# Performance work log

Measured on AMD Instinct MI355X. Metric: run time of the kernel, lower is better.

The kernel has to match this reference:

```python
import math
import jax, jax.numpy as jnp
import numpy as np

CH = 256
NUM_GROUPS = 32
EPS = 1e-5


def setup_inputs() -> dict:
    key = jax.random.key(0)
    ks = jax.random.split(key, 8)
    B, C, S = 32, CH, 32
    x = jax.random.normal(ks[0], (B, C, S, S), dtype=jnp.float32)
    t_embd = jax.random.normal(ks[1], (B, 4 * C), dtype=jnp.float32)
    gamma = jnp.ones((C,), dtype=jnp.float32)
    beta = jnp.zeros((C,), dtype=jnp.float32)
    # torch nn.Linear(ch, 3*ch): weight shape (3*ch, ch), y = x @ W.T + b
    w_attn = jax.random.normal(ks[2], (3 * C, C), dtype=jnp.float32) * (1.0 / math.sqrt(C))
    b_attn = jax.random.normal(ks[3], (3 * C,), dtype=jnp.float32) * 0.02
    w_proj = jax.random.normal(ks[4], (C, C), dtype=jnp.float32) * (1.0 / math.sqrt(C))
    b_proj = jax.random.normal(ks[5], (C,), dtype=jnp.float32) * 0.02
    return {
        "x": x, "t_embd": t_embd,
        "gamma": gamma, "beta": beta,
        "w_attn": w_attn, "b_attn": b_attn,
        "w_proj": w_proj, "b_proj": b_proj,
    }


def _group_norm(x, gamma, beta):
    # x: (B, C, S, S), normalize over (C/G, S, S) per group
    B, C, S, _ = x.shape
    xg = x.reshape(B, NUM_GROUPS, (C // NUM_GROUPS) * S * S)
    mean = jnp.mean(xg, axis=-1, keepdims=True)
    var = jnp.var(xg, axis=-1, keepdims=True)
    xn = ((xg - mean) * jax.lax.rsqrt(var + EPS)).reshape(B, C, S, S)
    return xn * gamma[None, :, None, None] + beta[None, :, None, None]


def reference(x, t_embd, gamma, beta, w_attn, b_attn, w_proj, b_proj):
    B, C, S, _ = x.shape
    norm_x = _group_norm(x, gamma, beta)
    h = jnp.transpose(norm_x, (0, 2, 3, 1))            # (B, S, S, C)
    qkv = h @ w_attn.T + b_attn                        # (B, S, S, 3C)
    q, k, v = jnp.split(qkv, 3, axis=3)
    # full spatial attention: scores over all S*S key positions
    att = jnp.einsum('bhwc,bHWc->bhwHW', q, k) * (1.0 / math.sqrt(C))
    att = jax.nn.softmax(att.reshape(B, S, S, S * S), axis=-1).reshape(B, S, S, S, S)
    o = jnp.einsum('bhwHW,bHWc->bhwc', att, v)         # (B, S, S, C)
    y = o @ w_proj.T + b_proj
    y = jnp.transpose(y, (0, 3, 1, 2))                 # (B, C, S, S)
    return x + y
```

## Files before the change

### kernel.cpp

```cpp
#include <hip/hip_runtime.h>
#include <hip/hip_bf16.h>
#include <stdint.h>
#include <stddef.h>


typedef float  f32x4  __attribute__((ext_vector_type(4)));
typedef __bf16 bf16x8 __attribute__((ext_vector_type(8)));
typedef __bf16 bf16x4 __attribute__((ext_vector_type(4)));

#define DEVI static __device__ __forceinline__

DEVI f32x4 mfma16(bf16x8 a, bf16x8 b, f32x4 c) {
  return __builtin_amdgcn_mfma_f32_16x16x32_bf16(a, b, c, 0, 0, 0);
}

DEVI f32x4 zero4() { f32x4 z = {0.f, 0.f, 0.f, 0.f}; return z; }

typedef const __attribute__((address_space(1))) void* gas_cvp;
typedef __attribute__((address_space(3))) void*       las_vp;

DEVI void gl_lds16(const __bf16* g, __bf16* l) {
  __builtin_amdgcn_global_load_lds((gas_cvp)g, (las_vp)l, 16, 0, 0);
}

#define WAIT_VM(N) asm volatile("s_waitcnt vmcnt(" #N ")" ::: "memory")
DEVI void bar() {
  asm volatile("" ::: "memory");
  __builtin_amdgcn_s_barrier();
  asm volatile("" ::: "memory");
}

__global__ __launch_bounds__(256) void cvt_weights(
    const float* __restrict__ wa, const float* __restrict__ wp,
    __bf16* __restrict__ wab, __bf16* __restrict__ wpb) {
  const int i = blockIdx.x * 256 + threadIdx.x;
  if (i < 196608) {
    wab[i] = (__bf16)wa[i];
  } else {
    const int j = i - 196608;
    if (j < 65536) wpb[j] = (__bf16)wp[j];
  }
}

__global__ __launch_bounds__(256) void gn_fused(
    const float* __restrict__ x, const float* __restrict__ gamma,
    const float* __restrict__ beta, __bf16* __restrict__ h) {
  __shared__ __align__(16) float xs[8192];
  __shared__ float redS[4], redSS[4];
  const int bg = blockIdx.x;
  const int b = bg >> 5, g = bg & 31;
  const int tid = threadIdx.x;
  const float* base = x + (size_t)bg * 8192;
  float s = 0.f, ss = 0.f;
#pragma unroll
  for (int it = 0; it < 8; ++it) {
    const int i = it * 256 + tid;
    f32x4 v = *(const f32x4*)(base + i * 4);
    *(f32x4*)(xs + i * 4) = v;
    s  += v[0] + v[1] + v[2] + v[3];
    ss += v[0]*v[0] + v[1]*v[1] + v[2]*v[2] + v[3]*v[3];
  }
#pragma unroll
  for (int m = 1; m < 64; m <<= 1) {
    s  += __shfl_xor(s,  m, 64);
    ss += __shfl_xor(ss, m, 64);
  }
  const int lane = tid & 63, wave = tid >> 6;
  if (lane == 0) { redS[wave] = s; redSS[wave] = ss; }
  __syncthreads();
  const float S  = redS[0] + redS[1] + redS[2] + redS[3];
  const float SS = redSS[0] + redSS[1] + redSS[2] + redSS[3];
  const float mu = S * (1.f / 8192.f);
  const float rstd = rsqrtf(SS * (1.f / 8192.f) - mu * mu + 1e-5f);
  float ga[8], be[8];
#pragma unroll
  for (int j = 0; j < 8; ++j) {
    const int c = g * 8 + j;
    ga[j] = gamma[c] * rstd;
    be[j] = beta[c] - mu * ga[j];
  }
  __bf16* hb = h + ((size_t)b << 18) + g * 8;
#pragma unroll
  for (int it = 0; it < 4; ++it) {
    const int p = it * 256 + tid;
    bf16x8 o8;
#pragma unroll
    for (int j = 0; j < 8; ++j)
      o8[j] = (__bf16)(xs[j * 1024 + p] * ga[j] + be[j]);
    *(bf16x8*)(hb + ((size_t)p << 8)) = o8;
  }
}

DEVI void gemm_core_k256(const __bf16* __restrict__ A0, const __bf16* __restrict__ B0,
                         __bf16* lA, __bf16* lB, int lane, int wave, f32x4 acc[4][4]) {
  const int wm = (wave >> 1) * 64;
  const int wn = (wave & 1) * 64;
  const int r15 = lane & 15, lg = lane >> 4;
#pragma unroll
  for (int i = 0; i < 4; ++i)
#pragma unroll
    for (int j = 0; j < 4; ++j) acc[i][j] = zero4();

  for (int ko = 0; ko < 4; ++ko) {
#pragma unroll
    for (int it = 0; it < 4; ++it) {
      const int q = wave * 256 + it * 64 + lane;
      const int row = q >> 3, c8 = q & 7;
      const int srcoff = row * 256 + ko * 64 + ((c8 ^ (row & 7)) << 3);
      gl_lds16(A0 + srcoff, lA + (size_t)(wave * 256 + it * 64) * 8);
      gl_lds16(B0 + srcoff, lB + (size_t)(wave * 256 + it * 64) * 8);
    }
    __syncthreads();
#pragma unroll
    for (int kk = 0; kk < 2; ++kk) {
      bf16x8 af[4], bfr[4];
#pragma unroll
      for (int i = 0; i < 4; ++i) {
        const int row = wm + i * 16 + r15;
        af[i] = *(const bf16x8*)((const char*)lA + row * 128 +
                                 (((kk * 4 + lg) ^ (row & 7)) << 4));
      }
#pragma unroll
      for (int j = 0; j < 4; ++j) {
        const int row = wn + j * 16 + r15;
        bfr[j] = *(const bf16x8*)((const char*)lB + row * 128 +
                                  (((kk * 4 + lg) ^ (row & 7)) << 4));
      }
#pragma unroll
      for (int i = 0; i < 4; ++i)
#pragma unroll
        for (int j = 0; j < 4; ++j) acc[i][j] = mfma16(af[i], bfr[j], acc[i][j]);
    }
    __syncthreads();
  }
}

__global__ __launch_bounds__(256) void qkv_gemm(
    const __bf16* __restrict__ h, const __bf16* __restrict__ wab,
    const float* __restrict__ b_attn,
    __bf16* __restrict__ q, __bf16* __restrict__ k, __bf16* __restrict__ vt) {
  __shared__ __align__(16) __bf16 lA[128 * 64], lB[128 * 64];
  const int nt = blockIdx.x, mt = blockIdx.y;
  const int tid = threadIdx.x, lane = tid & 63, wave = tid >> 6;
  f32x4 acc[4][4];
  gemm_core_k256(h + (size_t)mt * 128 * 256, wab + (size_t)nt * 128 * 256,
                 lA, lB, lane, wave, acc);

  const int wm = (wave >> 1) * 64, wn = (wave & 1) * 64;
  const int r15 = lane & 15, lg = lane >> 4;
  const int sec = nt >> 1;
  const float QS = 0.0625f * 1.44269504088896340736f;
#pragma unroll
  for (int j = 0; j < 4; ++j) {
    const int ng = nt * 128 + wn + j * 16 + r15;
    const float bias = b_attn[ng];
    const int c = ng & 255;
#pragma unroll
    for (int i = 0; i < 4; ++i) {
      const int mbase = mt * 128 + wm + i * 16 + lg * 4;
      if (sec == 0) {
#pragma unroll
        for (int r = 0; r < 4; ++r)
          q[(size_t)(mbase + r) * 256 + c] = (__bf16)((acc[i][j][r] + bias) * QS);
      } else if (sec == 1) {
#pragma unroll
        for (int r = 0; r < 4; ++r)
          k[(size_t)(mbase + r) * 256 + c] = (__bf16)(acc[i][j][r] + bias);
      } else {
        const int b = mbase >> 10, p = mbase & 1023;
        bf16x4 pk;
#pragma unroll
        for (int r = 0; r < 4; ++r) pk[r] = (__bf16)(acc[i][j][r] + bias);
        *(bf16x4*)(vt + (((size_t)(b * 256 + c)) << 10) + p) = pk;
      }
    }
  }
}

__global__ __launch_bounds__(256, 2) void attn(
    const __bf16* __restrict__ q, const __bf16* __restrict__ k,
    const __bf16* __restrict__ vt, __bf16* __restrict__ o) {
  extern __shared__ __align__(16) char smem[];

  const int bid = blockIdx.x;
  const int xcd = bid & 7, sub = bid >> 3;
  const int b = xcd * 4 + (sub & 3);
  const int qt = sub >> 2;
  const int tid = threadIdx.x, lane = tid & 63, wave = tid >> 6;
  const int r15 = lane & 15, lg = lane >> 4, rs7 = r15 & 7;
  const int m0 = qt * 64 + wave * 16;
  char* P = smem + 65536 + wave * 2048;

  const __bf16* kb = k  + ((size_t)b << 18);
  const __bf16* vb = vt + ((size_t)b << 18);

  const __bf16* qb = q + (((size_t)(b * 1024 + m0)) << 8);
  bf16x8 qf[8];
#pragma unroll
  for (int kc = 0; kc < 8; ++kc)
    qf[kc] = *(const bf16x8*)(qb + ((size_t)r15) * 256 + kc * 32 + lg * 8);

  f32x4 po[16];
#pragma unroll
  for (int d = 0; d < 16; ++d) po[d] = zero4();
  float mrun = -1e30f, lrun = 0.f;

  auto stageK = [&](int n0) {
    __bf16* dst = (__bf16*)smem;
#pragma unroll
    for (int it = 0; it < 8; ++it) {
      const int qch = it * 256 + tid;
      const int row = qch >> 5, c32 = qch & 31;
      gl_lds16(kb + (size_t)(n0 + row) * 256 + ((c32 ^ (row & 7)) << 3),
               dst + (size_t)(it * 256 + wave * 64) * 8);
    }
  };
  auto stageV = [&](int n0) {
    __bf16* dst = (__bf16*)(smem + 32768);
#pragma unroll
    for (int it = 0; it < 8; ++it) {
      const int qch = it * 256 + tid;
      const int row = qch >> 3, c8 = qch & 7;
      gl_lds16(vb + ((size_t)row << 10) + n0 + ((c8 ^ (row & 7)) << 3),
               dst + (size_t)(it * 256 + wave * 64) * 8);
    }
  };

  stageK(0);
  stageV(0);

  const char* lK = (const char*)smem;
  const char* lV = (const char*)smem + 32768;

  for (int kv = 0; kv < 16; ++kv) {
    WAIT_VM(8);
    bar();

    f32x4 s[4];
#pragma unroll
    for (int j = 0; j < 4; ++j) s[j] = zero4();
    __builtin_amdgcn_s_setprio(1);
#pragma unroll
    for (int kc = 0; kc < 8; ++kc) {
      bf16x8 kf[4];
#pragma unroll
      for (int j = 0; j < 4; ++j)
        kf[j] = *(const bf16x8*)(lK + (j * 16 + r15) * 512 +
                                 (((kc * 4 + lg) ^ rs7) << 4));
#pragma unroll
      for (int j = 0; j < 4; ++j) s[j] = mfma16(kf[j], qf[kc], s[j]);
    }
    __builtin_amdgcn_s_setprio(0);
    float pmax = s[0][0];
#pragma unroll
    for (int j = 0; j < 4; ++j)
#pragma unroll
      for (int r = 0; r < 4; ++r) pmax = fmaxf(pmax, s[j][r]);
    pmax = fmaxf(pmax, __shfl_xor(pmax, 16, 64));
    pmax = fmaxf(pmax, __shfl_xor(pmax, 32, 64));
    if (!__all(pmax <= mrun + 8.f)) {
      const float mn = fmaxf(mrun, pmax);
      const float scl = exp2f(mrun - mn);
      mrun = mn;
      lrun *= scl;
#pragma unroll
      for (int d = 0; d < 16; ++d) po[d] *= scl;
    }
    float psum = 0.f;
    bf16x4 pk[4];
#pragma unroll
    for (int j = 0; j < 4; ++j)
#pragma unroll
      for (int r = 0; r < 4; ++r) {
        const float pv = exp2f(s[j][r] - mrun);
        psum += pv;
        pk[j][r] = (__bf16)pv;
      }
    psum += __shfl_xor(psum, 16, 64);
    psum += __shfl_xor(psum, 32, 64);
    lrun += psum;
#pragma unroll
    for (int j = 0; j < 4; ++j)
      *(bf16x4*)(P + r15 * 128 + ((j * 32 + lg * 8) ^ (rs7 << 4))) = pk[j];

    WAIT_VM(0);
    bar();
    if (kv < 15) stageK((kv + 1) * 64);

    __builtin_amdgcn_s_setprio(1);
#pragma unroll
    for (int kk = 0; kk < 2; ++kk) {
      const bf16x8 pb =
          *(const bf16x8*)(P + r15 * 128 + (((kk * 4 + lg) ^ rs7) << 4));
#pragma unroll
      for (int df = 0; df < 16; ++df) {
        const bf16x8 vf = *(const bf16x8*)(lV + (df * 16 + r15) * 128 +
                                           (((kk * 4 + lg) ^ rs7) << 4));
        po[df] = mfma16(vf, pb, po[df]);
      }
    }
    __builtin_amdgcn_s_setprio(0);
    bar();
    if (kv < 15) stageV((kv + 1) * 64);
  }
  const float inv = 1.f / lrun;
  __bf16* ob = o + (((size_t)(b * 1024 + m0 + r15)) << 8);
#pragma unroll
  for (int df = 0; df < 16; ++df) {
    bf16x4 t;
#pragma unroll
    for (int r = 0; r < 4; ++r) t[r] = (__bf16)(po[df][r] * inv);
    *(bf16x4*)(ob + df * 16 + lg * 4) = t;
  }
}

__global__ __launch_bounds__(256) void proj_gemm(
    const __bf16* __restrict__ o, const __bf16* __restrict__ wpb,
    const float* __restrict__ b_proj, const float* __restrict__ x,
    float* __restrict__ out) {
  __shared__ __align__(16) __bf16 lA[128 * 64], lB[128 * 64];
  const int nt = blockIdx.x, mt = blockIdx.y;
  const int tid = threadIdx.x, lane = tid & 63, wave = tid >> 6;
  f32x4 acc[4][4];
  gemm_core_k256(o + (size_t)mt * 128 * 256, wpb + (size_t)nt * 128 * 256,
                 lA, lB, lane, wave, acc);

  const int wm = (wave >> 1) * 64, wn = (wave & 1) * 64;
  const int r15 = lane & 15, lg = lane >> 4;
#pragma unroll
  for (int j = 0; j < 4; ++j) {
    const int c = nt * 128 + wn + j * 16 + r15;
    const float bias = b_proj[c];
#pragma unroll
    for (int i = 0; i < 4; ++i) {
      const int mbase = mt * 128 + wm + i * 16 + lg * 4;
      const int b = mbase >> 10, p = mbase & 1023;
      const size_t off = (((size_t)(b * 256 + c)) << 10) + p;
      f32x4 xv = *(const f32x4*)(x + off);
      f32x4 r = acc[i][j];
      r = r + xv;
      r = r + bias;
      *(f32x4*)(out + off) = r;
    }
  }
}

extern "C" void kernel_launch(void* const* d_in, const int* in_sizes, int n_in,
                              void* d_out, int out_size, void* d_ws, size_t ws_size,
                              hipStream_t stream) {
  const float* x      = (const float*)d_in[0];
  const float* gamma  = (const float*)d_in[2];
  const float* beta   = (const float*)d_in[3];
  const float* w_attn = (const float*)d_in[4];
  const float* b_attn = (const float*)d_in[5];
  const float* w_proj = (const float*)d_in[6];
  const float* b_proj = (const float*)d_in[7];
  float* out = (float*)d_out;

  char* ws = (char*)d_ws;
  __bf16* h   = (__bf16*)(ws);
  __bf16* qb  = (__bf16*)(ws + ((size_t)16 << 20));
  __bf16* kb  = (__bf16*)(ws + ((size_t)32 << 20));
  __bf16* vtb = (__bf16*)(ws + ((size_t)48 << 20));
  __bf16* wab = (__bf16*)(ws + ((size_t)64 << 20));
  __bf16* wpb = wab + 196608;

  cvt_weights<<<1024, 256, 0, stream>>>(w_attn, w_proj, wab, wpb);
  gn_fused<<<1024, 256, 0, stream>>>(x, gamma, beta, h);
  qkv_gemm<<<dim3(6, 256), 256, 0, stream>>>(h, wab, b_attn, qb, kb, vtb);
  attn<<<512, 256, 73728, stream>>>(qb, kb, vtb, h );
  proj_gemm<<<dim3(2, 256), 256, 0, stream>>>(h, wpb, b_proj, x, out);
}
```

Before: 128.6 us.

## Split KV range across two wave groups per block with 32-row query tiles

```diff
diff --git a/kernel.cpp b/kernel.cpp
--- a/kernel.cpp
+++ b/kernel.cpp
@@ -177,7 +177,7 @@
   }
 }
 
-__global__ __launch_bounds__(256, 2) void attn(
+__global__ __launch_bounds__(512, 2) void attn(
     const __bf16* __restrict__ q, const __bf16* __restrict__ k,
     const __bf16* __restrict__ vt, __bf16* __restrict__ o) {
   extern __shared__ __align__(16) char smem[];
@@ -187,130 +187,178 @@
   const int b = xcd * 4 + (sub & 3);
   const int qt = sub >> 2;
   const int tid = threadIdx.x, lane = tid & 63, wave = tid >> 6;
+  const int w4 = wave & 3, grp = wave >> 2;
+  const int gtid = tid & 255;
   const int r15 = lane & 15, lg = lane >> 4, rs7 = r15 & 7;
-  const int m0 = qt * 64 + wave * 16;
-  char* P = smem + 65536 + wave * 2048;
+  const int m0 = qt * 128 + w4 * 32;
+  char* KB = smem + grp * 16384;
+  char* VB = smem + 32768 + grp * 16384;
+  char* P  = smem + 65536 + wave * 2048;
 
   const __bf16* kb = k  + ((size_t)b << 18);
   const __bf16* vb = vt + ((size_t)b << 18);
-
-  const __bf16* qb = q + (((size_t)(b * 1024 + m0)) << 8);
-  bf16x8 qf[8];
-#pragma unroll
-  for (int kc = 0; kc < 8; ++kc)
-    qf[kc] = *(const bf16x8*)(qb + ((size_t)r15) * 256 + kc * 32 + lg * 8);
-
-  f32x4 po[16];
-#pragma unroll
-  for (int d = 0; d < 16; ++d) po[d] = zero4();
-  float mrun = -1e30f, lrun = 0.f;
+  const int kvbase = grp * 512;
+
+  const __bf16* qbp = q + (((size_t)(b * 1024 + m0)) << 8);
+  bf16x8 qf[2][8];
+#pragma unroll
+  for (int qh = 0; qh < 2; ++qh)
+#pragma unroll
+    for (int kc = 0; kc < 8; ++kc)
+      qf[qh][kc] = *(const bf16x8*)(qbp + (size_t)(qh * 16 + r15) * 256 + kc * 32 + lg * 8);
+
+  f32x4 po[16][2];
+#pragma unroll
+  for (int d = 0; d < 16; ++d)
+#pragma unroll
+    for (int qh = 0; qh < 2; ++qh) po[d][qh] = zero4();
+  float mrun[2] = {-1e30f, -1e30f}, lrun[2] = {0.f, 0.f};
 
   auto stageK = [&](int n0) {
-    __bf16* dst = (__bf16*)smem;
-#pragma unroll
-    for (int it = 0; it < 8; ++it) {
-      const int qch = it * 256 + tid;
+    __bf16* dst = (__bf16*)KB;
+#pragma unroll
+    for (int it = 0; it < 4; ++it) {
+      const int qch = it * 256 + gtid;
       const int row = qch >> 5, c32 = qch & 31;
       gl_lds16(kb + (size_t)(n0 + row) * 256 + ((c32 ^ (row & 7)) << 3),
-               dst + (size_t)(it * 256 + wave * 64) * 8);
+               dst + (size_t)(it * 256 + w4 * 64) * 8);
     }
   };
   auto stageV = [&](int n0) {
-    __bf16* dst = (__bf16*)(smem + 32768);
-#pragma unroll
-    for (int it = 0; it < 8; ++it) {
-      const int qch = it * 256 + tid;
-      const int row = qch >> 3, c8 = qch & 7;
-      gl_lds16(vb + ((size_t)row << 10) + n0 + ((c8 ^ (row & 7)) << 3),
-               dst + (size_t)(it * 256 + wave * 64) * 8);
+    __bf16* dst = (__bf16*)VB;
+#pragma unroll
+    for (int it = 0; it < 4; ++it) {
+      const int qch = it * 256 + gtid;
+      const int row = qch >> 2, c4 = qch & 3;
+      gl_lds16(vb + ((size_t)row << 10) + n0 + ((c4 ^ (row & 3)) << 3),
+               dst + (size_t)(it * 256 + w4 * 64) * 8);
     }
   };
 
-  stageK(0);
-  stageV(0);
-
-  const char* lK = (const char*)smem;
-  const char* lV = (const char*)smem + 32768;
-
-  for (int kv = 0; kv < 16; ++kv) {
-    WAIT_VM(8);
+  stageK(kvbase);
+  stageV(kvbase);
+
+  for (int t = 0; t < 16; ++t) {
+    const int n0n = kvbase + (t + 1) * 32;
+    WAIT_VM(4);
     bar();
 
-    f32x4 s[4];
-#pragma unroll
-    for (int j = 0; j < 4; ++j) s[j] = zero4();
+    f32x4 s[2][2];
+#pragma unroll
+    for (int qh = 0; qh < 2; ++qh)
+#pragma unroll
+      for (int j = 0; j < 2; ++j) s[qh][j] = zero4();
     __builtin_amdgcn_s_setprio(1);
 #pragma unroll
     for (int kc = 0; kc < 8; ++kc) {
-      bf16x8 kf[4];
-#pragma unroll
-      for (int j = 0; j < 4; ++j)
-        kf[j] = *(const bf16x8*)(lK + (j * 16 + r15) * 512 +
+      bf16x8 kf[2];
+#pragma unroll
+      for (int j = 0; j < 2; ++j)
+        kf[j] = *(const bf16x8*)(KB + (j * 16 + r15) * 512 +
                                  (((kc * 4 + lg) ^ rs7) << 4));
 #pragma unroll
-      for (int j = 0; j < 4; ++j) s[j] = mfma16(kf[j], qf[kc], s[j]);
+      for (int qh = 0; qh < 2; ++qh)
+#pragma unroll
+        for (int j = 0; j < 2; ++j) s[qh][j] = mfma16(kf[j], qf[qh][kc], s[qh][j]);
     }
     __builtin_amdgcn_s_setprio(0);
-    float pmax = s[0][0];
-#pragma unroll
-    for (int j = 0; j < 4; ++j)
-#pragma unroll
-      for (int r = 0; r < 4; ++r) pmax = fmaxf(pmax, s[j][r]);
-    pmax = fmaxf(pmax, __shfl_xor(pmax, 16, 64));
-    pmax = fmaxf(pmax, __shfl_xor(pmax, 32, 64));
-    if (!__all(pmax <= mrun + 8.f)) {
-      const float mn = fmaxf(mrun, pmax);
-      const float scl = exp2f(mrun - mn);
-      mrun = mn;
-      lrun *= scl;
-#pragma unroll
-      for (int d = 0; d < 16; ++d) po[d] *= scl;
-    }
-    float psum = 0.f;
-    bf16x4 pk[4];
-#pragma unroll
-    for (int j = 0; j < 4; ++j)
-#pragma unroll
-      for (int r = 0; r < 4; ++r) {
-        const float pv = exp2f(s[j][r] - mrun);
-        psum += pv;
-        pk[j][r] = (__bf16)pv;
-      }
-    psum += __shfl_xor(psum, 16, 64);
-    psum += __shfl_xor(psum, 32, 64);
-    lrun += psum;
-#pragma unroll
-    for (int j = 0; j < 4; ++j)
-      *(bf16x4*)(P + r15 * 128 + ((j * 32 + lg * 8) ^ (rs7 << 4))) = pk[j];
+    bf16x4 pk[2][2];
+#pragma unroll
+    for (int qh = 0; qh < 2; ++qh) {
+      float pmax = s[qh][0][0];
+#pragma unroll
+      for (int j = 0; j < 2; ++j)
+#pragma unroll
+        for (int r = 0; r < 4; ++r) pmax = fmaxf(pmax, s[qh][j][r]);
+      pmax = fmaxf(pmax, __shfl_xor(pmax, 16, 64));
+      pmax = fmaxf(pmax, __shfl_xor(pmax, 32, 64));
+      if (!__all(pmax <= mrun[qh] + 8.f)) {
+        const float mn = fmaxf(mrun[qh], pmax);
+        const float scl = exp2f(mrun[qh] - mn);
+        mrun[qh] = mn;
+        lrun[qh] *= scl;
+#pragma unroll
+        for (int d = 0; d < 16; ++d) po[d][qh] *= scl;
+      }
+      float psum = 0.f;
+#pragma unroll
+      for (int j = 0; j < 2; ++j)
+#pragma unroll
+        for (int r = 0; r < 4; ++r) {
+          const float pv = exp2f(s[qh][j][r] - mrun[qh]);
+          psum += pv;
+          pk[qh][j][r] = (__bf16)pv;
+        }
+      psum += __shfl_xor(psum, 16, 64);
+      psum += __shfl_xor(psum, 32, 64);
+      lrun[qh] += psum;
+    }
+#pragma unroll
+    for (int qh = 0; qh < 2; ++qh)
+#pragma unroll
+      for (int j = 0; j < 2; ++j) {
+        const int prow = qh * 16 + r15;
+        const int slot = (j * 2 + (lg >> 1)) ^ (prow & 3);
+        *(bf16x4*)(P + prow * 64 + (slot << 4) + ((lg & 1) * 8)) = pk[qh][j];
+      }
 
     WAIT_VM(0);
     bar();
-    if (kv < 15) stageK((kv + 1) * 64);
-
+    if (t < 15) stageK(n0n);
+
+    bf16x8 pb[2];
+#pragma unroll
+    for (int qh = 0; qh < 2; ++qh) {
+      const int prow = qh * 16 + r15;
+      pb[qh] = *(const bf16x8*)(P + prow * 64 + ((lg ^ (prow & 3)) << 4));
+    }
     __builtin_amdgcn_s_setprio(1);
 #pragma unroll
-    for (int kk = 0; kk < 2; ++kk) {
-      const bf16x8 pb =
-          *(const bf16x8*)(P + r15 * 128 + (((kk * 4 + lg) ^ rs7) << 4));
-#pragma unroll
-      for (int df = 0; df < 16; ++df) {
-        const bf16x8 vf = *(const bf16x8*)(lV + (df * 16 + r15) * 128 +
-                                           (((kk * 4 + lg) ^ rs7) << 4));
-        po[df] = mfma16(vf, pb, po[df]);
-      }
+    for (int df = 0; df < 16; ++df) {
+      const int vrow = df * 16 + r15;
+      const bf16x8 vf = *(const bf16x8*)(VB + vrow * 64 + ((lg ^ (vrow & 3)) << 4));
+#pragma unroll
+      for (int qh = 0; qh < 2; ++qh) po[df][qh] = mfma16(vf, pb[qh], po[df][qh]);
     }
     __builtin_amdgcn_s_setprio(0);
     bar();
-    if (kv < 15) stageV((kv + 1) * 64);
-  }
-  const float inv = 1.f / lrun;
-  __bf16* ob = o + (((size_t)(b * 1024 + m0 + r15)) << 8);
-#pragma unroll
-  for (int df = 0; df < 16; ++df) {
-    bf16x4 t;
-#pragma unroll
-    for (int r = 0; r < 4; ++r) t[r] = (__bf16)(po[df][r] * inv);
-    *(bf16x4*)(ob + df * 16 + lg * 4) = t;
+    if (t < 15) stageV(n0n);
+  }
+
+  if (grp == 1) {
+    f32x4 ml = {mrun[0], mrun[1], lrun[0], lrun[1]};
+    *(f32x4*)(smem + 65536 + ((w4 * 64 + lane) << 4)) = ml;
+#pragma unroll
+    for (int qh = 0; qh < 2; ++qh)
+#pragma unroll
+      for (int df = 0; df < 16; ++df) {
+        bf16x4 t;
+#pragma unroll
+        for (int r = 0; r < 4; ++r) t[r] = (__bf16)(po[df][qh][r]);
+        *(bf16x4*)(smem + w4 * 16384 + (qh * 16 + df) * 512 + lane * 8) = t;
+      }
+  }
+  bar();
+  if (grp == 0) {
+    const f32x4 ml = *(const f32x4*)(smem + 65536 + ((w4 * 64 + lane) << 4));
+#pragma unroll
+    for (int qh = 0; qh < 2; ++qh) {
+      const float m1 = ml[qh], l1 = ml[2 + qh];
+      const float M = fmaxf(mrun[qh], m1);
+      const float a0 = exp2f(mrun[qh] - M), a1 = exp2f(m1 - M);
+      const float inv = 1.f / (a0 * lrun[qh] + a1 * l1);
+      __bf16* ob = o + (((size_t)(b * 1024 + m0 + qh * 16 + r15)) << 8);
+#pragma unroll
+      for (int df = 0; df < 16; ++df) {
+        const bf16x4 p1 =
+            *(const bf16x4*)(smem + w4 * 16384 + (qh * 16 + df) * 512 + lane * 8);
+        bf16x4 t;
+#pragma unroll
+        for (int r = 0; r < 4; ++r)
+          t[r] = (__bf16)((a0 * po[df][qh][r] + a1 * (float)p1[r]) * inv);
+        *(bf16x4*)(ob + df * 16 + lg * 4) = t;
+      }
+    }
   }
 }
 
@@ -368,6 +416,6 @@
   cvt_weights<<<1024, 256, 0, stream>>>(w_attn, w_proj, wab, wpb);
   gn_fused<<<1024, 256, 0, stream>>>(x, gamma, beta, h);
   qkv_gemm<<<dim3(6, 256), 256, 0, stream>>>(h, wab, b_attn, qb, kb, vtb);
-  attn<<<512, 256, 73728, stream>>>(qb, kb, vtb, h );
+  attn<<<256, 512, 81920, stream>>>(qb, kb, vtb, h );
   proj_gemm<<<dim3(2, 256), 256, 0, stream>>>(h, wpb, b_proj, x, out);
 }
```

After: 142.6 us. +10.9%, slower.

## Split PV output across waves by head-dim slice with shared P tile

Applied to the files above, without the earlier changes.

```diff
diff --git a/kernel.cpp b/kernel.cpp
--- a/kernel.cpp
+++ b/kernel.cpp
@@ -177,7 +177,7 @@
   }
 }
 
-__global__ __launch_bounds__(256, 2) void attn(
+__global__ __launch_bounds__(256, 1) void attn(
     const __bf16* __restrict__ q, const __bf16* __restrict__ k,
     const __bf16* __restrict__ vt, __bf16* __restrict__ o) {
   extern __shared__ __align__(16) char smem[];
@@ -188,25 +188,31 @@
   const int qt = sub >> 2;
   const int tid = threadIdx.x, lane = tid & 63, wave = tid >> 6;
   const int r15 = lane & 15, lg = lane >> 4, rs7 = r15 & 7;
-  const int m0 = qt * 64 + wave * 16;
-  char* P = smem + 65536 + wave * 2048;
+  const int m0 = qt * 64;
+  char* lK = smem;
+  char* lV = smem + 32768;
+  char* P  = smem + 65536;
+  float* sclb = (float*)(smem + 73728);
+  float* lfin = (float*)(smem + 73984);
 
   const __bf16* kb = k  + ((size_t)b << 18);
   const __bf16* vb = vt + ((size_t)b << 18);
 
-  const __bf16* qb = q + (((size_t)(b * 1024 + m0)) << 8);
+  const __bf16* qbp = q + (((size_t)(b * 1024 + m0 + wave * 16)) << 8);
   bf16x8 qf[8];
 #pragma unroll
   for (int kc = 0; kc < 8; ++kc)
-    qf[kc] = *(const bf16x8*)(qb + ((size_t)r15) * 256 + kc * 32 + lg * 8);
-
-  f32x4 po[16];
-#pragma unroll
-  for (int d = 0; d < 16; ++d) po[d] = zero4();
+    qf[kc] = *(const bf16x8*)(qbp + ((size_t)r15) * 256 + kc * 32 + lg * 8);
+
+  f32x4 po[4][4];
+#pragma unroll
+  for (int df = 0; df < 4; ++df)
+#pragma unroll
+    for (int qf2 = 0; qf2 < 4; ++qf2) po[df][qf2] = zero4();
   float mrun = -1e30f, lrun = 0.f;
 
   auto stageK = [&](int n0) {
-    __bf16* dst = (__bf16*)smem;
+    __bf16* dst = (__bf16*)lK;
 #pragma unroll
     for (int it = 0; it < 8; ++it) {
       const int qch = it * 256 + tid;
@@ -216,7 +222,7 @@
     }
   };
   auto stageV = [&](int n0) {
-    __bf16* dst = (__bf16*)(smem + 32768);
+    __bf16* dst = (__bf16*)lV;
 #pragma unroll
     for (int it = 0; it < 8; ++it) {
       const int qch = it * 256 + tid;
@@ -229,10 +235,8 @@
   stageK(0);
   stageV(0);
 
-  const char* lK = (const char*)smem;
-  const char* lV = (const char*)smem + 32768;
-
-  for (int kv = 0; kv < 16; ++kv) {
+  for (int t = 0; t < 16; ++t) {
+    const int n0n = (t + 1) * 64;
     WAIT_VM(8);
     bar();
 
@@ -258,13 +262,12 @@
       for (int r = 0; r < 4; ++r) pmax = fmaxf(pmax, s[j][r]);
     pmax = fmaxf(pmax, __shfl_xor(pmax, 16, 64));
     pmax = fmaxf(pmax, __shfl_xor(pmax, 32, 64));
+    float sclv = 1.f;
     if (!__all(pmax <= mrun + 8.f)) {
       const float mn = fmaxf(mrun, pmax);
-      const float scl = exp2f(mrun - mn);
+      sclv = exp2f(mrun - mn);
       mrun = mn;
-      lrun *= scl;
-#pragma unroll
-      for (int d = 0; d < 16; ++d) po[d] *= scl;
+      lrun *= sclv;
     }
     float psum = 0.f;
     bf16x4 pk[4];
@@ -279,38 +282,68 @@
     psum += __shfl_xor(psum, 16, 64);
     psum += __shfl_xor(psum, 32, 64);
     lrun += psum;
-#pragma unroll
-    for (int j = 0; j < 4; ++j)
-      *(bf16x4*)(P + r15 * 128 + ((j * 32 + lg * 8) ^ (rs7 << 4))) = pk[j];
+    {
+      const int prow = wave * 16 + r15;
+#pragma unroll
+      for (int j = 0; j < 4; ++j)
+        *(bf16x4*)(P + prow * 128 + ((j * 32 + lg * 8) ^ (rs7 << 4))) = pk[j];
+      if (lg == 0) sclb[prow] = sclv;
+    }
 
     WAIT_VM(0);
     bar();
-    if (kv < 15) stageK((kv + 1) * 64);
-
+    if (t < 15) stageK(n0n);
+
+    {
+      float sv[4];
+#pragma unroll
+      for (int qf2 = 0; qf2 < 4; ++qf2) sv[qf2] = sclb[qf2 * 16 + r15];
+      if (!__all(sv[0] * sv[1] * sv[2] * sv[3] == 1.f)) {
+#pragma unroll
+        for (int df = 0; df < 4; ++df)
+#pragma unroll
+          for (int qf2 = 0; qf2 < 4; ++qf2) po[df][qf2] *= sv[qf2];
+      }
+    }
+    bf16x8 pb[4][2];
+#pragma unroll
+    for (int qf2 = 0; qf2 < 4; ++qf2)
+#pragma unroll
+      for (int kk = 0; kk < 2; ++kk)
+        pb[qf2][kk] = *(const bf16x8*)(P + (qf2 * 16 + r15) * 128 +
+                                       (((kk * 4 + lg) ^ rs7) << 4));
     __builtin_amdgcn_s_setprio(1);
 #pragma unroll
-    for (int kk = 0; kk < 2; ++kk) {
-      const bf16x8 pb =
-          *(const bf16x8*)(P + r15 * 128 + (((kk * 4 + lg) ^ rs7) << 4));
-#pragma unroll
-      for (int df = 0; df < 16; ++df) {
-        const bf16x8 vf = *(const bf16x8*)(lV + (df * 16 + r15) * 128 +
+    for (int df = 0; df < 4; ++df)
+#pragma unroll
+      for (int kk = 0; kk < 2; ++kk) {
+        const int vrow = wave * 64 + df * 16 + r15;
+        const bf16x8 vf = *(const bf16x8*)(lV + vrow * 128 +
                                            (((kk * 4 + lg) ^ rs7) << 4));
-        po[df] = mfma16(vf, pb, po[df]);
-      }
-    }
+#pragma unroll
+        for (int qf2 = 0; qf2 < 4; ++qf2)
+          po[df][qf2] = mfma16(vf, pb[qf2][kk], po[df][qf2]);
+      }
     __builtin_amdgcn_s_setprio(0);
     bar();
-    if (kv < 15) stageV((kv + 1) * 64);
-  }
-  const float inv = 1.f / lrun;
-  __bf16* ob = o + (((size_t)(b * 1024 + m0 + r15)) << 8);
-#pragma unroll
-  for (int df = 0; df < 16; ++df) {
-    bf16x4 t;
-#pragma unroll
-    for (int r = 0; r < 4; ++r) t[r] = (__bf16)(po[df][r] * inv);
-    *(bf16x4*)(ob + df * 16 + lg * 4) = t;
+    if (t < 15) stageV(n0n);
+  }
+
+  if (lg == 0) lfin[wave * 16 + r15] = lrun;
+  __syncthreads();
+  float inv[4];
+#pragma unroll
+  for (int qf2 = 0; qf2 < 4; ++qf2) inv[qf2] = 1.f / lfin[qf2 * 16 + r15];
+#pragma unroll
+  for (int qf2 = 0; qf2 < 4; ++qf2) {
+    __bf16* ob = o + (((size_t)(b * 1024 + m0 + qf2 * 16 + r15)) << 8) + wave * 64;
+#pragma unroll
+    for (int df = 0; df < 4; ++df) {
+      bf16x4 tv;
+#pragma unroll
+      for (int r = 0; r < 4; ++r) tv[r] = (__bf16)(po[df][qf2][r] * inv[qf2]);
+      *(bf16x4*)(ob + df * 16 + lg * 4) = tv;
+    }
   }
 }
 
@@ -368,6 +401,6 @@
   cvt_weights<<<1024, 256, 0, stream>>>(w_attn, w_proj, wab, wpb);
   gn_fused<<<1024, 256, 0, stream>>>(x, gamma, beta, h);
   qkv_gemm<<<dim3(6, 256), 256, 0, stream>>>(h, wab, b_attn, qb, kb, vtb);
-  attn<<<512, 256, 73728, stream>>>(qb, kb, vtb, h );
+  attn<<<512, 256, 74240, stream>>>(qb, kb, vtb, h );
   proj_gemm<<<dim3(2, 256), 256, 0, stream>>>(h, wpb, b_proj, x, out);
 }
```

Result: slower. 149.0 us (+15.9%).

## Fuse weight conversion into groupnorm launch and widen QKV GEMM N-tile

Applied to the files above, without the earlier changes.

```diff
diff --git a/kernel.cpp b/kernel.cpp
--- a/kernel.cpp
+++ b/kernel.cpp
@@ -30,26 +30,22 @@
   asm volatile("" ::: "memory");
 }
 
-__global__ __launch_bounds__(256) void cvt_weights(
+__global__ __launch_bounds__(256) void gn_fused(
+    const float* __restrict__ x, const float* __restrict__ gamma,
+    const float* __restrict__ beta, __bf16* __restrict__ h,
     const float* __restrict__ wa, const float* __restrict__ wp,
     __bf16* __restrict__ wab, __bf16* __restrict__ wpb) {
-  const int i = blockIdx.x * 256 + threadIdx.x;
-  if (i < 196608) {
-    wab[i] = (__bf16)wa[i];
-  } else {
-    const int j = i - 196608;
-    if (j < 65536) wpb[j] = (__bf16)wp[j];
-  }
-}
-
-__global__ __launch_bounds__(256) void gn_fused(
-    const float* __restrict__ x, const float* __restrict__ gamma,
-    const float* __restrict__ beta, __bf16* __restrict__ h) {
   __shared__ __align__(16) float xs[8192];
   __shared__ float redS[4], redSS[4];
+  const int tid = threadIdx.x;
+  if (blockIdx.x >= 1024) {
+    const int i = (blockIdx.x - 1024) * 256 + tid;
+    if (i < 196608) wab[i] = (__bf16)wa[i];
+    else wpb[i - 196608] = (__bf16)wp[i - 196608];
+    return;
+  }
   const int bg = blockIdx.x;
   const int b = bg >> 5, g = bg & 31;
-  const int tid = threadIdx.x;
   const float* base = x + (size_t)bg * 8192;
   float s = 0.f, ss = 0.f;
 #pragma unroll
@@ -91,29 +87,43 @@
   }
 }
 
-DEVI void gemm_core_k256(const __bf16* __restrict__ A0, const __bf16* __restrict__ B0,
-                         __bf16* lA, __bf16* lB, int lane, int wave, f32x4 acc[4][4]) {
-  const int wm = (wave >> 1) * 64;
-  const int wn = (wave & 1) * 64;
+__global__ __launch_bounds__(256) void qkv_gemm(
+    const __bf16* __restrict__ h, const __bf16* __restrict__ wab,
+    const float* __restrict__ b_attn,
+    __bf16* __restrict__ q, __bf16* __restrict__ k, __bf16* __restrict__ vt) {
+  __shared__ __align__(16) __bf16 lA[128 * 64], lB[256 * 64];
+  const int nt = blockIdx.x, mt = blockIdx.y;
+  const int tid = threadIdx.x, lane = tid & 63, wave = tid >> 6;
+  const int wm = (wave >> 1) * 64, wn = (wave & 1) * 128;
   const int r15 = lane & 15, lg = lane >> 4;
+  const __bf16* A0 = h + (size_t)mt * 128 * 256;
+  const __bf16* B0 = wab + (size_t)nt * 256 * 256;
+
+  f32x4 acc[4][8];
 #pragma unroll
   for (int i = 0; i < 4; ++i)
 #pragma unroll
-    for (int j = 0; j < 4; ++j) acc[i][j] = zero4();
+    for (int j = 0; j < 8; ++j) acc[i][j] = zero4();
 
   for (int ko = 0; ko < 4; ++ko) {
 #pragma unroll
     for (int it = 0; it < 4; ++it) {
-      const int q = wave * 256 + it * 64 + lane;
-      const int row = q >> 3, c8 = q & 7;
-      const int srcoff = row * 256 + ko * 64 + ((c8 ^ (row & 7)) << 3);
-      gl_lds16(A0 + srcoff, lA + (size_t)(wave * 256 + it * 64) * 8);
-      gl_lds16(B0 + srcoff, lB + (size_t)(wave * 256 + it * 64) * 8);
+      const int q8 = it * 256 + tid;
+      const int row = q8 >> 3, c8 = q8 & 7;
+      gl_lds16(A0 + row * 256 + ko * 64 + ((c8 ^ (row & 7)) << 3),
+               lA + (size_t)(it * 256 + wave * 64) * 8);
+    }
+#pragma unroll
+    for (int it = 0; it < 8; ++it) {
+      const int q8 = it * 256 + tid;
+      const int row = q8 >> 3, c8 = q8 & 7;
+      gl_lds16(B0 + row * 256 + ko * 64 + ((c8 ^ (row & 7)) << 3),
+               lB + (size_t)(it * 256 + wave * 64) * 8);
     }
     __syncthreads();
 #pragma unroll
     for (int kk = 0; kk < 2; ++kk) {
-      bf16x8 af[4], bfr[4];
+      bf16x8 af[4], bfr[8];
 #pragma unroll
       for (int i = 0; i < 4; ++i) {
         const int row = wm + i * 16 + r15;
@@ -121,7 +131,7 @@
                                  (((kk * 4 + lg) ^ (row & 7)) << 4));
       }
 #pragma unroll
-      for (int j = 0; j < 4; ++j) {
+      for (int j = 0; j < 8; ++j) {
         const int row = wn + j * 16 + r15;
         bfr[j] = *(const bf16x8*)((const char*)lB + row * 128 +
                                   (((kk * 4 + lg) ^ (row & 7)) << 4));
@@ -129,40 +139,24 @@
 #pragma unroll
       for (int i = 0; i < 4; ++i)
 #pragma unroll
-        for (int j = 0; j < 4; ++j) acc[i][j] = mfma16(af[i], bfr[j], acc[i][j]);
+        for (int j = 0; j < 8; ++j) acc[i][j] = mfma16(af[i], bfr[j], acc[i][j]);
     }
     __syncthreads();
   }
-}
-
-__global__ __launch_bounds__(256) void qkv_gemm(
-    const __bf16* __restrict__ h, const __bf16* __restrict__ wab,
-    const float* __restrict__ b_attn,
-    __bf16* __restrict__ q, __bf16* __restrict__ k, __bf16* __restrict__ vt) {
-  __shared__ __align__(16) __bf16 lA[128 * 64], lB[128 * 64];
-  const int nt = blockIdx.x, mt = blockIdx.y;
-  const int tid = threadIdx.x, lane = tid & 63, wave = tid >> 6;
-  f32x4 acc[4][4];
-  gemm_core_k256(h + (size_t)mt * 128 * 256, wab + (size_t)nt * 128 * 256,
-                 lA, lB, lane, wave, acc);
-
-  const int wm = (wave >> 1) * 64, wn = (wave & 1) * 64;
-  const int r15 = lane & 15, lg = lane >> 4;
-  const int sec = nt >> 1;
+
   const float QS = 0.0625f * 1.44269504088896340736f;
 #pragma unroll
-  for (int j = 0; j < 4; ++j) {
-    const int ng = nt * 128 + wn + j * 16 + r15;
-    const float bias = b_attn[ng];
-    const int c = ng & 255;
+  for (int j = 0; j < 8; ++j) {
+    const int c = wn + j * 16 + r15;
+    const float bias = b_attn[nt * 256 + c];
 #pragma unroll
     for (int i = 0; i < 4; ++i) {
       const int mbase = mt * 128 + wm + i * 16 + lg * 4;
-      if (sec == 0) {
+      if (nt == 0) {
 #pragma unroll
         for (int r = 0; r < 4; ++r)
           q[(size_t)(mbase + r) * 256 + c] = (__bf16)((acc[i][j][r] + bias) * QS);
-      } else if (sec == 1) {
+      } else if (nt == 1) {
 #pragma unroll
         for (int r = 0; r < 4; ++r)
           k[(size_t)(mbase + r) * 256 + c] = (__bf16)(acc[i][j][r] + bias);
@@ -311,6 +305,50 @@
 #pragma unroll
     for (int r = 0; r < 4; ++r) t[r] = (__bf16)(po[df][r] * inv);
     *(bf16x4*)(ob + df * 16 + lg * 4) = t;
+  }
+}
+
+DEVI void gemm_core_k256(const __bf16* __restrict__ A0, const __bf16* __restrict__ B0,
+                         __bf16* lA, __bf16* lB, int lane, int wave, f32x4 acc[4][4]) {
+  const int wm = (wave >> 1) * 64;
+  const int wn = (wave & 1) * 64;
+  const int r15 = lane & 15, lg = lane >> 4;
+#pragma unroll
+  for (int i = 0; i < 4; ++i)
+#pragma unroll
+    for (int j = 0; j < 4; ++j) acc[i][j] = zero4();
+
+  for (int ko = 0; ko < 4; ++ko) {
+#pragma unroll
+    for (int it = 0; it < 4; ++it) {
+      const int q = wave * 256 + it * 64 + lane;
+      const int row = q >> 3, c8 = q & 7;
+      const int srcoff = row * 256 + ko * 64 + ((c8 ^ (row & 7)) << 3);
+      gl_lds16(A0 + srcoff, lA + (size_t)(wave * 256 + it * 64) * 8);
+      gl_lds16(B0 + srcoff, lB + (size_t)(wave * 256 + it * 64) * 8);
+    }
+    __syncthreads();
+#pragma unroll
+    for (int kk = 0; kk < 2; ++kk) {
+      bf16x8 af[4], bfr[4];
+#pragma unroll
+      for (int i = 0; i < 4; ++i) {
+        const int row = wm + i * 16 + r15;
+        af[i] = *(const bf16x8*)((const char*)lA + row * 128 +
+                                 (((kk * 4 + lg) ^ (row & 7)) << 4));
+      }
+#pragma unroll
+      for (int j = 0; j < 4; ++j) {
+        const int row = wn + j * 16 + r15;
+        bfr[j] = *(const bf16x8*)((const char*)lB + row * 128 +
+                                  (((kk * 4 + lg) ^ (row & 7)) << 4));
+      }
+#pragma unroll
+      for (int i = 0; i < 4; ++i)
+#pragma unroll
+        for (int j = 0; j < 4; ++j) acc[i][j] = mfma16(af[i], bfr[j], acc[i][j]);
+    }
+    __syncthreads();
   }
 }
 
@@ -365,9 +403,8 @@
   __bf16* wab = (__bf16*)(ws + ((size_t)64 << 20));
   __bf16* wpb = wab + 196608;
 
-  cvt_weights<<<1024, 256, 0, stream>>>(w_attn, w_proj, wab, wpb);
-  gn_fused<<<1024, 256, 0, stream>>>(x, gamma, beta, h);
-  qkv_gemm<<<dim3(6, 256), 256, 0, stream>>>(h, wab, b_attn, qb, kb, vtb);
+  gn_fused<<<2048, 256, 0, stream>>>(x, gamma, beta, h, w_attn, w_proj, wab, wpb);
+  qkv_gemm<<<dim3(3, 256), 256, 0, stream>>>(h, wab, b_attn, qb, kb, vtb);
   attn<<<512, 256, 73728, stream>>>(qb, kb, vtb, h );
   proj_gemm<<<dim3(2, 256), 256, 0, stream>>>(h, wpb, b_proj, x, out);
 }
```

Result: slower. 134.2 us (+4.4%).
